# Optimization experiments

Hardware: AMD Instinct MI355X
Metric: run time of the kernel (lower is better)

## Reference

```python
import jax, jax.numpy as jnp
import numpy as np

B, S, H, M, E = 64, 512, 1024, 26, 676  # batch, seq, hidden, max_nodes, max_edges (M*M)


def setup_inputs() -> dict:
    key = jax.random.key(0)
    ks = jax.random.split(key, 16)
    seq = jax.random.normal(ks[0], (B, S, H), jnp.float32)
    # ragged, strictly-increasing sentence-end offsets in [1, S-1], zero-padded tail
    rng = np.random.RandomState(0)
    off = np.zeros((B, M - 1), np.int64)
    for b in range(B):
        c = rng.randint(5, M)  # count of valid offsets per sample (ragged)
        off[b, :c] = np.sort(rng.choice(np.arange(1, S), size=c, replace=False))
    s = 1.0 / np.sqrt(H)
    s3 = 1.0 / np.sqrt(3 * H)
    return {
        'sequence_outputs': seq,
        'proof_offsets': jnp.asarray(off),
        'node_labels': jax.random.randint(ks[1], (B, M), 0, 2),
        'edge_labels': jax.random.randint(ks[2], (B, E), 0, 2),
        'W_naf': jax.random.normal(ks[3], (H, H), jnp.float32) * s,
        'b_naf': jnp.zeros((H,), jnp.float32),
        'W_cd': jax.random.normal(ks[4], (H, H), jnp.float32) * s,
        'b_cd': jnp.zeros((H,), jnp.float32),
        'W_co': jax.random.normal(ks[5], (H, 2), jnp.float32) * s,
        'b_co': jnp.zeros((2,), jnp.float32),
        'W_nd': jax.random.normal(ks[6], (H, H), jnp.float32) * s,
        'b_nd': jnp.zeros((H,), jnp.float32),
        'W_no': jax.random.normal(ks[7], (H, 2), jnp.float32) * s,
        'b_no': jnp.zeros((2,), jnp.float32),
        'W_ed': jax.random.normal(ks[8], (3 * H, H), jnp.float32) * s3,
        'b_ed': jnp.zeros((H,), jnp.float32),
        'W_eo': jax.random.normal(ks[9], (H, 2), jnp.float32) * s,
        'b_eo': jnp.zeros((2,), jnp.float32),
    }


def reference(sequence_outputs, proof_offsets, node_labels, edge_labels,
              W_naf, b_naf, W_cd, b_cd, W_co, b_co,
              W_nd, b_nd, W_no, b_no, W_ed, b_ed, W_eo, b_eo):
    Bx, Sx, Hx = sequence_outputs.shape
    Mx = node_labels.shape[1]
    Ex = edge_labels.shape[1]

    cls = sequence_outputs[:, 0, :]                       # [B,H]
    naf = cls @ W_naf + b_naf                             # NAF node embedding
    logits = jnp.tanh(cls @ W_cd + b_cd) @ W_co + b_co    # RobertaClassificationHead (eval: dropout=id)

    # segment-mean pooling via inclusive prefix sums: segment j = tokens (prev_j, off_j]
    P = jnp.cumsum(sequence_outputs, axis=1)              # [B,S,H]
    off = proof_offsets                                   # [B,M-1]
    prev = jnp.concatenate([jnp.zeros((Bx, 1), off.dtype), off[:, :-1]], axis=1)
    valid = off > 0                                       # [B,M-1]
    seg_sum = (jnp.take_along_axis(P, off[..., None], axis=1)
               - jnp.take_along_axis(P, prev[..., None], axis=1))  # [B,M-1,H]
    seg_len = jnp.maximum(off - prev, 1).astype(sequence_outputs.dtype)
    seg_mean = seg_sum / seg_len[..., None] * valid[..., None]

    count = valid.sum(axis=1)                             # nodes per sample (excl. NAF)
    # node embeddings: seg means at 0..count-1, NAF at index count, zeros after
    node_full = jnp.concatenate([seg_mean, jnp.zeros((Bx, 1, Hx), seg_mean.dtype)], axis=1)  # [B,M,H]
    idx = jnp.arange(Mx)
    node_full = node_full + (idx[None, :, None] == count[:, None, None]) * naf[:, None, :]

    # all-pairs edge features over n=count+1 nodes, row-major flat k=i*n+j, zero-padded to E
    n = count + 1                                         # [B]
    k = jnp.arange(Ex)                                    # [E]
    i = jnp.clip(k[None, :] // n[:, None], 0, Mx - 1)     # [B,E]
    j = jnp.clip(k[None, :] % n[:, None], 0, Mx - 1)
    valid_e = (k[None, :] < (n * n)[:, None])[..., None]
    ni = jnp.take_along_axis(node_full, i[..., None], axis=1)  # [B,E,H]
    nj = jnp.take_along_axis(node_full, j[..., None], axis=1)
    edge = jnp.concatenate([nj, ni, nj - ni], axis=-1) * valid_e  # [B,E,3H]

    node_logits = jnp.tanh(node_full @ W_nd + b_nd) @ W_no + b_no
    edge_logits = jnp.tanh(edge @ W_ed + b_ed) @ W_eo + b_eo
    return (logits, node_logits, edge_logits)
```

## Files before the change

kernel.cpp:

```cpp
#include <hip/hip_runtime.h>
#include <hip/hip_bf16.h>

#define B_ 64
#define S_ 512
#define H_ 1024
#define M_ 26
#define E_ 676

typedef short bf16x8 __attribute__((ext_vector_type(8)));
typedef float f32x4 __attribute__((ext_vector_type(4)));

__device__ __forceinline__ void gload16(const void* g, void* l) {
    __builtin_amdgcn_global_load_lds((const __attribute__((address_space(1))) unsigned int*)g,
                                     (__attribute__((address_space(3))) unsigned int*)l,
                                     16, 0, 0);
}

__device__ __forceinline__ float tanh_fast(float x) {
    float e = __expf(2.0f * x);
    return 1.0f - 2.0f * __builtin_amdgcn_rcpf(e + 1.0f);
}

__global__ __launch_bounds__(256) void k_segk(const float* __restrict__ seq,
                                              const int* __restrict__ off,
                                              float* __restrict__ node_sum) {
    __shared__ int offs[32];
    __shared__ int cs[2];
    int bid = blockIdx.x;
    int tid = threadIdx.x;
    int chunk = bid & 31, b = bid >> 5;
    if (tid < M_ - 1) offs[tid] = off[b * (M_ - 1) + tid];
    __syncthreads();
    if (tid == 0) {
        int c = 0;
        while (c < M_ - 1 && offs[c] > 0) c++;
        cs[0] = c; cs[1] = (c > 0) ? offs[c - 1] : 0;
    }
    __syncthreads();
    int c = cs[0], offmax = cs[1];
    int t0 = chunk * 16;
    int ts = max(t0, 1), te = min(t0 + 15, offmax);
    if (ts > te) return;
    int m = 0;
    while (m < c && offs[m] < ts) m++;
    const float4* sq = (const float4*)(seq + (size_t)b * S_ * H_) + tid;
    int t = ts;
    while (t <= te) {
        int segEnd = min(offs[m], te);
        int L = segEnd - t + 1;
        const float4* p = sq + (size_t)t * (H_ / 4);
        float4 a0 = make_float4(0, 0, 0, 0);
        float4 a1 = a0, a2 = a0, a3 = a0;
        int u = 0;
        for (; u + 4 <= L; u += 4) {
            float4 v0 = p[(size_t)(u + 0) * (H_ / 4)];
            float4 v1 = p[(size_t)(u + 1) * (H_ / 4)];
            float4 v2 = p[(size_t)(u + 2) * (H_ / 4)];
            float4 v3 = p[(size_t)(u + 3) * (H_ / 4)];
            a0.x += v0.x; a0.y += v0.y; a0.z += v0.z; a0.w += v0.w;
            a1.x += v1.x; a1.y += v1.y; a1.z += v1.z; a1.w += v1.w;
            a2.x += v2.x; a2.y += v2.y; a2.z += v2.z; a2.w += v2.w;
            a3.x += v3.x; a3.y += v3.y; a3.z += v3.z; a3.w += v3.w;
        }
        for (; u < L; ++u) {
            float4 v0 = p[(size_t)u * (H_ / 4)];
            a0.x += v0.x; a0.y += v0.y; a0.z += v0.z; a0.w += v0.w;
        }
        a0.x += a1.x + a2.x + a3.x;
        a0.y += a1.y + a2.y + a3.y;
        a0.z += a1.z + a2.z + a3.z;
        a0.w += a1.w + a2.w + a3.w;
        float* dst = node_sum + ((size_t)(b * M_ + m)) * H_ + tid * 4;
        atomicAdd(dst + 0, a0.x); atomicAdd(dst + 1, a0.y);
        atomicAdd(dst + 2, a0.z); atomicAdd(dst + 3, a0.w);
        t = segEnd + 1;
        m++;
    }
}

__global__ __launch_bounds__(256) void k_aux(
    const float* __restrict__ seq, const int* __restrict__ off,
    const float* __restrict__ Wnaf, const float* __restrict__ Wcd,
    const float* __restrict__ Wnd, const float* __restrict__ Wed,
    const float* __restrict__ bed, const float* __restrict__ Weo,
    const float* __restrict__ beo,
    __hip_bfloat16* __restrict__ Wt, int* __restrict__ count,
    float* __restrict__ econ, float* __restrict__ naf, float* __restrict__ cdh) {
    __shared__ float smem[2112];
    int bid = blockIdx.x;
    int tid = threadIdx.x;
    if (bid < 256) {
        float (*As)[64] = (float(*)[64])smem;
        float (*Bs)[64] = (float(*)[64])(smem + 1024);
        int bx = bid & 31;
        int kbase = (bid >> 5) * 128;
        const float* W;
        float* dst;
        int cbase;
        if (bx < 16) { W = Wnaf; dst = naf; cbase = bx * 64; }
        else         { W = Wcd;  dst = cdh; cbase = (bx - 16) * 64; }
        int tx = tid % 16, ty = tid / 16;
        float c[4][4] = {};
        int la_row = tid / 4;
        int la_k4  = (tid % 4) * 4;
        int lb_k   = tid / 16;
        int lb_c4  = (tid % 16) * 4;
        for (int k0 = 0; k0 < 128; k0 += 16) {
            float4 a = *(const float4*)(seq + (size_t)la_row * S_ * H_ + kbase + k0 + la_k4);
            *(float4*)(&Bs[lb_k][lb_c4]) =
                *(const float4*)(W + (size_t)(kbase + k0 + lb_k) * H_ + cbase + lb_c4);
            As[la_k4 + 0][la_row] = a.x;
            As[la_k4 + 1][la_row] = a.y;
            As[la_k4 + 2][la_row] = a.z;
            As[la_k4 + 3][la_row] = a.w;
            __syncthreads();
#pragma unroll
            for (int kk = 0; kk < 16; ++kk) {
                float4 av = *(const float4*)(&As[kk][ty * 4]);
                float4 bv = *(const float4*)(&Bs[kk][tx * 4]);
                c[0][0] += av.x * bv.x; c[0][1] += av.x * bv.y; c[0][2] += av.x * bv.z; c[0][3] += av.x * bv.w;
                c[1][0] += av.y * bv.x; c[1][1] += av.y * bv.y; c[1][2] += av.y * bv.z; c[1][3] += av.y * bv.w;
                c[2][0] += av.z * bv.x; c[2][1] += av.z * bv.y; c[2][2] += av.z * bv.z; c[2][3] += av.z * bv.w;
                c[3][0] += av.w * bv.x; c[3][1] += av.w * bv.y; c[3][2] += av.w * bv.z; c[3][3] += av.w * bv.w;
            }
            __syncthreads();
        }
#pragma unroll
        for (int i = 0; i < 4; ++i)
#pragma unroll
            for (int j = 0; j < 4; ++j)
                atomicAdd(dst + (size_t)(ty * 4 + i) * H_ + cbase + tx * 4 + j, c[i][j]);
    } else if (bid < 1280) {
        float (*T1)[33] = (float(*)[33])smem;
        float (*T2)[33] = (float(*)[33])(smem + 1056);
        int e = bid - 256;
        int bx = e & 31, by = e >> 5;
        int cc = tid & 31, r0 = tid >> 5;
        const int HH = H_ * H_;
#pragma unroll
        for (int i = 0; i < 4; ++i) {
            int r = r0 + 8 * i;
            size_t k = by * 32 + r, n = bx * 32 + cc;
            float w1 = Wed[k * H_ + n];
            float w2 = Wed[HH + k * H_ + n];
            float w3 = Wed[2 * HH + k * H_ + n];
            T1[r][cc] = w1 + w3;
            T2[r][cc] = w2 - w3;
        }
        __syncthreads();
#pragma unroll
        for (int i = 0; i < 4; ++i) {
            int rr = r0 + 8 * i;
            Wt[(size_t)(H_ + bx * 32 + rr) * H_ + by * 32 + cc]     = __float2bfloat16(T1[cc][rr]);
            Wt[(size_t)(2 * H_ + bx * 32 + rr) * H_ + by * 32 + cc] = __float2bfloat16(T2[cc][rr]);
        }
    } else if (bid < 2304) {
        float (*T)[33] = (float(*)[33])smem;
        int e = bid - 1280;
        int bx = e & 31, by = e >> 5;
        int cc = tid & 31, r0 = tid >> 5;
#pragma unroll
        for (int i = 0; i < 4; ++i) {
            int r = r0 + 8 * i;
            size_t k = by * 32 + r, n = bx * 32 + cc;
            T[r][cc] = Wnd[k * H_ + n];
        }
        __syncthreads();
#pragma unroll
        for (int i = 0; i < 4; ++i) {
            int rr = r0 + 8 * i;
            Wt[(size_t)(bx * 32 + rr) * H_ + by * 32 + cc] = __float2bfloat16(T[cc][rr]);
        }
    } else if (bid == 2304) {
        if (tid < 64) {
            int b = tid;
            int c = 0;
            for (int m = 0; m < M_ - 1; ++m) c += (off[b * (M_ - 1) + m] > 0) ? 1 : 0;
            count[b] = c;
        }
    } else {
        float* s0 = smem; float* s1 = smem + 256;
        float a0 = 0.f, a1 = 0.f;
        for (int h = tid; h < H_; h += 256) {
            float t = tanh_fast(bed[h]);
            a0 += t * Weo[h * 2 + 0];
            a1 += t * Weo[h * 2 + 1];
        }
        s0[tid] = a0; s1[tid] = a1; __syncthreads();
        for (int o = 128; o > 0; o >>= 1) {
            if (tid < o) { s0[tid] += s0[tid + o]; s1[tid] += s1[tid + o]; }
            __syncthreads();
        }
        if (tid == 0) { econ[0] = s0[0] + beo[0]; econ[1] = s1[0] + beo[1]; }
    }
}

__global__ __launch_bounds__(256) void k_stage2(
    const float* __restrict__ sums, const int* __restrict__ off,
    const int* __restrict__ count, const float* __restrict__ naf,
    const float* __restrict__ bnaf, __hip_bfloat16* __restrict__ nodeB,
    const float* __restrict__ cdh, const float* __restrict__ bcd,
    const float* __restrict__ Wco, const float* __restrict__ bco,
    float* __restrict__ out) {
    __shared__ float smem[512];
    int bid = blockIdx.x;
    int tid = threadIdx.x;
    if (bid < 1664) {
        int b = bid / 26, m = bid - b * 26;
        int cnt = count[b];
        float4 v = make_float4(0, 0, 0, 0);
        const float4* row = (const float4*)(sums + ((size_t)(b * M_ + m)) * H_);
        if (m < M_ - 1) {
            int o = off[b * (M_ - 1) + m];
            if (o > 0) {
                int prev = (m > 0) ? off[b * (M_ - 1) + m - 1] : 0;
                float inv = 1.0f / (float)max(o - prev, 1);
                float4 s = row[tid];
                v = make_float4(s.x * inv, s.y * inv, s.z * inv, s.w * inv);
            }
        }
        if (m == cnt) {
            float4 a = ((const float4*)(naf + (size_t)b * H_))[tid];
            float4 bb = ((const float4*)bnaf)[tid];
            v.x += a.x + bb.x; v.y += a.y + bb.y; v.z += a.z + bb.z; v.w += a.w + bb.w;
        }
        __hip_bfloat16 __attribute__((aligned(8))) h[4] = {
            __float2bfloat16(v.x), __float2bfloat16(v.y),
            __float2bfloat16(v.z), __float2bfloat16(v.w)};
        *(ushort4*)(nodeB + ((size_t)(b * M_ + m)) * H_ + tid * 4) = *(const ushort4*)h;
    } else {
        int b = bid - 1664;
        float* s0 = smem; float* s1 = smem + 256;
        float a0 = 0.f, a1 = 0.f;
        for (int h = tid; h < H_; h += 256) {
            float t = tanh_fast(cdh[(size_t)b * H_ + h] + bcd[h]);
            a0 += t * Wco[h * 2 + 0];
            a1 += t * Wco[h * 2 + 1];
        }
        s0[tid] = a0; s1[tid] = a1; __syncthreads();
        for (int o = 128; o > 0; o >>= 1) {
            if (tid < o) { s0[tid] += s0[tid + o]; s1[tid] += s1[tid + o]; }
            __syncthreads();
        }
        if (tid == 0) { out[b * 2 + 0] = s0[0] + bco[0]; out[b * 2 + 1] = s1[0] + bco[1]; }
    }
}

#define GM 1664
#define GN 3072
#define GK 1024
__global__ __launch_bounds__(256) void k_mfma(const __hip_bfloat16* __restrict__ A,
                                              const __hip_bfloat16* __restrict__ Bt,
                                              float* __restrict__ C) {
    __shared__ __hip_bfloat16 As[128 * 32];
    __shared__ __hip_bfloat16 Bs[128 * 32];
    int tid = threadIdx.x;
    int wid = tid >> 6, ln = tid & 63;
    int row0 = blockIdx.y * 128, col0 = blockIdx.x * 128;
    const __hip_bfloat16* ga = A + (size_t)(row0 + wid * 16 + (ln >> 2)) * GK + (ln & 3) * 8;
    const __hip_bfloat16* gb = Bt + (size_t)(col0 + wid * 16 + (ln >> 2)) * GK + (ln & 3) * 8;
    __hip_bfloat16* lA = As + wid * 512;
    __hip_bfloat16* lB = Bs + wid * 512;
    int mrow = (wid >> 1) * 64, ncol = (wid & 1) * 64;
    int l15 = ln & 15, l4 = ln >> 4;
    f32x4 acc[4][4] = {};
    const __hip_bfloat16* pa = As + (size_t)(mrow + l15) * 32 + l4 * 8;
    const __hip_bfloat16* pb = Bs + (size_t)(ncol + l15) * 32 + l4 * 8;
    for (int k0 = 0; k0 < GK; k0 += 32) {
        gload16(ga, lA);
        gload16(ga + 64 * GK, lA + 2048);
        gload16(gb, lB);
        gload16(gb + 64 * GK, lB + 2048);
        ga += 32; gb += 32;
        __syncthreads();
        bf16x8 af[4], bf[4];
#pragma unroll
        for (int mi = 0; mi < 4; ++mi) af[mi] = *(const bf16x8*)(pa + mi * 16 * 32);
#pragma unroll
        for (int ni = 0; ni < 4; ++ni) bf[ni] = *(const bf16x8*)(pb + ni * 16 * 32);
#pragma unroll
        for (int mi = 0; mi < 4; ++mi)
#pragma unroll
            for (int ni = 0; ni < 4; ++ni)
                acc[mi][ni] = __builtin_amdgcn_mfma_f32_16x16x32_bf16(af[mi], bf[ni],
                                                                      acc[mi][ni], 0, 0, 0);
        __syncthreads();
    }
#pragma unroll
    for (int mi = 0; mi < 4; ++mi)
#pragma unroll
        for (int ni = 0; ni < 4; ++ni) {
            f32x4 v = acc[mi][ni];
            size_t r = row0 + mrow + mi * 16 + l4 * 4;
            size_t cc = col0 + ncol + ni * 16 + l15;
            C[(r + 0) * GN + cc] = v[0];
            C[(r + 1) * GN + cc] = v[1];
            C[(r + 2) * GN + cc] = v[2];
            C[(r + 3) * GN + cc] = v[3];
        }
}

__global__ __launch_bounds__(256) void k_stage4(
    const float* __restrict__ Cm, const int* __restrict__ count,
    const float* __restrict__ bnd, const float* __restrict__ Wno,
    const float* __restrict__ bno, const float* __restrict__ bed,
    const float* __restrict__ Weo, const float* __restrict__ beo,
    const float* __restrict__ econ, float* __restrict__ out_n,
    float* __restrict__ out_e) {
    int bid = blockIdx.x;
    int wid = threadIdx.x >> 6, lane = threadIdx.x & 63;
    if (bid < 416) {
        int r = bid * 4 + wid;
        const float4* src = (const float4*)(Cm + (size_t)r * GN);
        float a0 = 0.f, a1 = 0.f;
#pragma unroll
        for (int it = 0; it < 4; ++it) {
            int h = lane * 4 + it * 256;
            float4 s = src[lane + it * 64];
            float4 bb = *(const float4*)(bnd + h);
            float t0 = tanh_fast(s.x + bb.x), t1 = tanh_fast(s.y + bb.y);
            float t2 = tanh_fast(s.z + bb.z), t3 = tanh_fast(s.w + bb.w);
            a0 += t0 * Wno[h * 2 + 0] + t1 * Wno[h * 2 + 2] + t2 * Wno[h * 2 + 4] + t3 * Wno[h * 2 + 6];
            a1 += t0 * Wno[h * 2 + 1] + t1 * Wno[h * 2 + 3] + t2 * Wno[h * 2 + 5] + t3 * Wno[h * 2 + 7];
        }
        for (int o = 32; o > 0; o >>= 1) { a0 += __shfl_down(a0, o); a1 += __shfl_down(a1, o); }
        if (lane == 0) { out_n[(size_t)r * 2 + 0] = a0 + bno[0]; out_n[(size_t)r * 2 + 1] = a1 + bno[1]; }
    } else {
        int e = bid - 416;
        int b = e >> 4;
        int wg = (e & 15) * 4 + wid;
        int n = count[b] + 1;
        int n2 = n * n;
        float4 bed4[4], w04[4], w14[4];
#pragma unroll
        for (int it = 0; it < 4; ++it) {
            int h = lane * 4 + it * 256;
            bed4[it] = *(const float4*)(bed + h);
            w04[it] = make_float4(Weo[h * 2 + 0], Weo[h * 2 + 2], Weo[h * 2 + 4], Weo[h * 2 + 6]);
            w14[it] = make_float4(Weo[h * 2 + 1], Weo[h * 2 + 3], Weo[h * 2 + 5], Weo[h * 2 + 7]);
        }
        float e0 = econ[0], e1 = econ[1];
        float b0 = beo[0], b1 = beo[1];
        for (int k = wg; k < E_; k += 64) {
            float* dst = out_e + ((size_t)b * E_ + k) * 2;
            if (k >= n2) {
                if (lane == 0) { dst[0] = e0; dst[1] = e1; }
                continue;
            }
            int i = k / n, j = k - i * n;
            const float4* U4 = (const float4*)(Cm + (size_t)(b * M_ + j) * GN + H_);
            const float4* V4 = (const float4*)(Cm + (size_t)(b * M_ + i) * GN + 2 * H_);
            float a0 = 0.f, a1 = 0.f;
#pragma unroll
            for (int it = 0; it < 4; ++it) {
                float4 u = U4[lane + it * 64];
                float4 v = V4[lane + it * 64];
                float t0 = tanh_fast(u.x + v.x + bed4[it].x);
                float t1 = tanh_fast(u.y + v.y + bed4[it].y);
                float t2 = tanh_fast(u.z + v.z + bed4[it].z);
                float t3 = tanh_fast(u.w + v.w + bed4[it].w);
                a0 += t0 * w04[it].x + t1 * w04[it].y + t2 * w04[it].z + t3 * w04[it].w;
                a1 += t0 * w14[it].x + t1 * w14[it].y + t2 * w14[it].z + t3 * w14[it].w;
            }
            for (int o = 32; o > 0; o >>= 1) { a0 += __shfl_down(a0, o); a1 += __shfl_down(a1, o); }
            if (lane == 0) { dst[0] = a0 + b0; dst[1] = a1 + b1; }
        }
    }
}

extern "C" void kernel_launch(void* const* d_in, const int* in_sizes, int n_in,
                              void* d_out, int out_size, void* d_ws, size_t ws_size,
                              hipStream_t stream) {
    const float* seq  = (const float*)d_in[0];
    const int*   off  = (const int*)d_in[1];
    const float* Wnaf = (const float*)d_in[4];  const float* bnaf = (const float*)d_in[5];
    const float* Wcd  = (const float*)d_in[6];  const float* bcd  = (const float*)d_in[7];
    const float* Wco  = (const float*)d_in[8];  const float* bco  = (const float*)d_in[9];
    const float* Wnd  = (const float*)d_in[10]; const float* bnd  = (const float*)d_in[11];
    const float* Wno  = (const float*)d_in[12]; const float* bno  = (const float*)d_in[13];
    const float* Wed  = (const float*)d_in[14]; const float* bed  = (const float*)d_in[15];
    const float* Weo  = (const float*)d_in[16]; const float* beo  = (const float*)d_in[17];
    float* out = (float*)d_out;

    float* ws = (float*)d_ws;
    size_t p = 0;
    float* nodeS = ws + p;  p += (size_t)B_ * M_ * H_;
    float* naf   = ws + p;  p += (size_t)B_ * H_;
    float* cdh   = ws + p;  p += (size_t)B_ * H_;
    __hip_bfloat16* nodeB = (__hip_bfloat16*)(ws + p); p += (size_t)B_ * M_ * H_ / 2;
    __hip_bfloat16* Wt    = (__hip_bfloat16*)(ws + p); p += (size_t)3 * H_ * H_ / 2;
    float* Cbuf  = ws + p;  p += (size_t)B_ * M_ * 3 * H_;
    int*   cnt   = (int*)(ws + p); p += 64;
    float* econ  = ws + p;  p += 2;

    hipMemsetAsync(nodeS, 0, ((size_t)B_ * M_ * H_ + 2 * (size_t)B_ * H_) * sizeof(float),
                   stream);

    k_segk<<<dim3(2048), 256, 0, stream>>>(seq, off, nodeS);
    k_aux<<<dim3(2306), 256, 0, stream>>>(seq, off, Wnaf, Wcd, Wnd, Wed, bed, Weo, beo,
                                          Wt, cnt, econ, naf, cdh);
    k_stage2<<<dim3(1728), 256, 0, stream>>>(nodeS, off, cnt, naf, bnaf, nodeB,
                                             cdh, bcd, Wco, bco, out);
    k_mfma<<<dim3(GN / 128, GM / 128), 256, 0, stream>>>(nodeB, Wt, Cbuf);
    k_stage4<<<dim3(1440), 256, 0, stream>>>(Cbuf, cnt, bnd, Wno, bno, bed, Weo, beo, econ,
                                             out + B_ * 2, out + B_ * 2 + B_ * M_ * 2);
}
```

Baseline: 333.4 us.

## Fuse segment-sum pooling into node finalization kernel, drop atomics and node-sum buffer

Removes the separate chunked segment-sum kernel, which accumulated token rows into a zeroed fp32 node-sum buffer with atomics. Each node block now reads its segment's rows from the sequence directly, sums them with an 8-way unrolled loop, divides by the length and writes bf16. This drops the large memset, one launch, the atomics and a write-then-read round trip of the intermediate buffer. In exchange, work per block is uneven because segment lengths vary, so a single long segment is reduced by one block with less parallelism than the chunked version had.

```diff
diff --git a/kernel.cpp b/kernel.cpp
--- a/kernel.cpp
+++ b/kernel.cpp
@@ -19,63 +19,6 @@
 __device__ __forceinline__ float tanh_fast(float x) {
     float e = __expf(2.0f * x);
     return 1.0f - 2.0f * __builtin_amdgcn_rcpf(e + 1.0f);
-}
-
-__global__ __launch_bounds__(256) void k_segk(const float* __restrict__ seq,
-                                              const int* __restrict__ off,
-                                              float* __restrict__ node_sum) {
-    __shared__ int offs[32];
-    __shared__ int cs[2];
-    int bid = blockIdx.x;
-    int tid = threadIdx.x;
-    int chunk = bid & 31, b = bid >> 5;
-    if (tid < M_ - 1) offs[tid] = off[b * (M_ - 1) + tid];
-    __syncthreads();
-    if (tid == 0) {
-        int c = 0;
-        while (c < M_ - 1 && offs[c] > 0) c++;
-        cs[0] = c; cs[1] = (c > 0) ? offs[c - 1] : 0;
-    }
-    __syncthreads();
-    int c = cs[0], offmax = cs[1];
-    int t0 = chunk * 16;
-    int ts = max(t0, 1), te = min(t0 + 15, offmax);
-    if (ts > te) return;
-    int m = 0;
-    while (m < c && offs[m] < ts) m++;
-    const float4* sq = (const float4*)(seq + (size_t)b * S_ * H_) + tid;
-    int t = ts;
-    while (t <= te) {
-        int segEnd = min(offs[m], te);
-        int L = segEnd - t + 1;
-        const float4* p = sq + (size_t)t * (H_ / 4);
-        float4 a0 = make_float4(0, 0, 0, 0);
-        float4 a1 = a0, a2 = a0, a3 = a0;
-        int u = 0;
-        for (; u + 4 <= L; u += 4) {
-            float4 v0 = p[(size_t)(u + 0) * (H_ / 4)];
-            float4 v1 = p[(size_t)(u + 1) * (H_ / 4)];
-            float4 v2 = p[(size_t)(u + 2) * (H_ / 4)];
-            float4 v3 = p[(size_t)(u + 3) * (H_ / 4)];
-            a0.x += v0.x; a0.y += v0.y; a0.z += v0.z; a0.w += v0.w;
-            a1.x += v1.x; a1.y += v1.y; a1.z += v1.z; a1.w += v1.w;
-            a2.x += v2.x; a2.y += v2.y; a2.z += v2.z; a2.w += v2.w;
-            a3.x += v3.x; a3.y += v3.y; a3.z += v3.z; a3.w += v3.w;
-        }
-        for (; u < L; ++u) {
-            float4 v0 = p[(size_t)u * (H_ / 4)];
-            a0.x += v0.x; a0.y += v0.y; a0.z += v0.z; a0.w += v0.w;
-        }
-        a0.x += a1.x + a2.x + a3.x;
-        a0.y += a1.y + a2.y + a3.y;
-        a0.z += a1.z + a2.z + a3.z;
-        a0.w += a1.w + a2.w + a3.w;
-        float* dst = node_sum + ((size_t)(b * M_ + m)) * H_ + tid * 4;
-        atomicAdd(dst + 0, a0.x); atomicAdd(dst + 1, a0.y);
-        atomicAdd(dst + 2, a0.z); atomicAdd(dst + 3, a0.w);
-        t = segEnd + 1;
-        m++;
-    }
 }
 
 __global__ __launch_bounds__(256) void k_aux(
@@ -195,8 +138,8 @@
     }
 }
 
-__global__ __launch_bounds__(256) void k_stage2(
-    const float* __restrict__ sums, const int* __restrict__ off,
+__global__ __launch_bounds__(256) void k_segfin(
+    const float* __restrict__ seq, const int* __restrict__ off,
     const int* __restrict__ count, const float* __restrict__ naf,
     const float* __restrict__ bnaf, __hip_bfloat16* __restrict__ nodeB,
     const float* __restrict__ cdh, const float* __restrict__ bcd,
@@ -209,20 +152,42 @@
         int b = bid / 26, m = bid - b * 26;
         int cnt = count[b];
         float4 v = make_float4(0, 0, 0, 0);
-        const float4* row = (const float4*)(sums + ((size_t)(b * M_ + m)) * H_);
-        if (m < M_ - 1) {
-            int o = off[b * (M_ - 1) + m];
-            if (o > 0) {
-                int prev = (m > 0) ? off[b * (M_ - 1) + m - 1] : 0;
-                float inv = 1.0f / (float)max(o - prev, 1);
-                float4 s = row[tid];
-                v = make_float4(s.x * inv, s.y * inv, s.z * inv, s.w * inv);
-            }
-        }
-        if (m == cnt) {
+        if (m < cnt) {
+            int hi = off[b * (M_ - 1) + m];
+            int lo = (m > 0 ? off[b * (M_ - 1) + m - 1] : 0) + 1;
+            int L = hi - lo + 1;
+            const float4* p = (const float4*)(seq + (size_t)b * S_ * H_) +
+                              (size_t)lo * (H_ / 4) + tid;
+            float4 a0 = make_float4(0, 0, 0, 0);
+            float4 a1 = a0, a2 = a0, a3 = a0;
+            int u = 0;
+            for (; u + 8 <= L; u += 8) {
+                float4 v0 = p[(size_t)(u + 0) * (H_ / 4)];
+                float4 v1 = p[(size_t)(u + 1) * (H_ / 4)];
+                float4 v2 = p[(size_t)(u + 2) * (H_ / 4)];
+                float4 v3 = p[(size_t)(u + 3) * (H_ / 4)];
+                float4 v4 = p[(size_t)(u + 4) * (H_ / 4)];
+                float4 v5 = p[(size_t)(u + 5) * (H_ / 4)];
+                float4 v6 = p[(size_t)(u + 6) * (H_ / 4)];
+                float4 v7 = p[(size_t)(u + 7) * (H_ / 4)];
+                a0.x += v0.x + v4.x; a0.y += v0.y + v4.y; a0.z += v0.z + v4.z; a0.w += v0.w + v4.w;
+                a1.x += v1.x + v5.x; a1.y += v1.y + v5.y; a1.z += v1.z + v5.z; a1.w += v1.w + v5.w;
+                a2.x += v2.x + v6.x; a2.y += v2.y + v6.y; a2.z += v2.z + v6.z; a2.w += v2.w + v6.w;
+                a3.x += v3.x + v7.x; a3.y += v3.y + v7.y; a3.z += v3.z + v7.z; a3.w += v3.w + v7.w;
+            }
+            for (; u < L; ++u) {
+                float4 v0 = p[(size_t)u * (H_ / 4)];
+                a0.x += v0.x; a0.y += v0.y; a0.z += v0.z; a0.w += v0.w;
+            }
+            float inv = 1.0f / (float)L;
+            v.x = (a0.x + a1.x + a2.x + a3.x) * inv;
+            v.y = (a0.y + a1.y + a2.y + a3.y) * inv;
+            v.z = (a0.z + a1.z + a2.z + a3.z) * inv;
+            v.w = (a0.w + a1.w + a2.w + a3.w) * inv;
+        } else if (m == cnt) {
             float4 a = ((const float4*)(naf + (size_t)b * H_))[tid];
             float4 bb = ((const float4*)bnaf)[tid];
-            v.x += a.x + bb.x; v.y += a.y + bb.y; v.z += a.z + bb.z; v.w += a.w + bb.w;
+            v.x = a.x + bb.x; v.y = a.y + bb.y; v.z = a.z + bb.z; v.w = a.w + bb.w;
         }
         __hip_bfloat16 __attribute__((aligned(8))) h[4] = {
             __float2bfloat16(v.x), __float2bfloat16(v.y),
@@ -384,7 +349,6 @@
 
     float* ws = (float*)d_ws;
     size_t p = 0;
-    float* nodeS = ws + p;  p += (size_t)B_ * M_ * H_;
     float* naf   = ws + p;  p += (size_t)B_ * H_;
     float* cdh   = ws + p;  p += (size_t)B_ * H_;
     __hip_bfloat16* nodeB = (__hip_bfloat16*)(ws + p); p += (size_t)B_ * M_ * H_ / 2;
@@ -393,13 +357,11 @@
     int*   cnt   = (int*)(ws + p); p += 64;
     float* econ  = ws + p;  p += 2;
 
-    hipMemsetAsync(nodeS, 0, ((size_t)B_ * M_ * H_ + 2 * (size_t)B_ * H_) * sizeof(float),
-                   stream);
-
-    k_segk<<<dim3(2048), 256, 0, stream>>>(seq, off, nodeS);
+    hipMemsetAsync(naf, 0, (size_t)2 * B_ * H_ * sizeof(float), stream);
+
     k_aux<<<dim3(2306), 256, 0, stream>>>(seq, off, Wnaf, Wcd, Wnd, Wed, bed, Weo, beo,
                                           Wt, cnt, econ, naf, cdh);
-    k_stage2<<<dim3(1728), 256, 0, stream>>>(nodeS, off, cnt, naf, bnaf, nodeB,
+    k_segfin<<<dim3(1728), 256, 0, stream>>>(seq, off, cnt, naf, bnaf, nodeB,
                                              cdh, bcd, Wco, bco, out);
     k_mfma<<<dim3(GN / 128, GM / 128), 256, 0, stream>>>(nodeB, Wt, Cbuf);
     k_stage4<<<dim3(1440), 256, 0, stream>>>(Cbuf, cnt, bnd, Wno, bno, bed, Weo, beo, econ,
```

Result: no change. 331.3 us (-0.6%).
